# Kernel tuning notes

Hardware: AMD Instinct MI355X
Metric: run time of the kernel (lower is better)

Reference implementation:

```python
import jax, jax.numpy as jnp
import numpy as np

SCALE = 32.0 / 32.0  # alpha / rank
KEEP = 1.0 - 0.05    # dropout keep prob


def setup_inputs() -> dict:
    key = jax.random.key(0)
    kx, kw, ka, kb, km = jax.random.split(key, 5)
    B_, S, D_in, D_out, R = 4, 2048, 4096, 4096, 32
    x = jax.random.normal(kx, (B_, S, D_in), dtype=jnp.float32)
    W = jax.random.normal(kw, (D_out, D_in), dtype=jnp.float32) * (1.0 / np.sqrt(D_in))
    A = jax.random.normal(ka, (D_in, R), dtype=jnp.float32) * (1.0 / np.sqrt(D_in))
    Bm = jax.random.normal(kb, (R, D_out), dtype=jnp.float32) * 0.02
    # deterministic inverted-dropout mask: {0, 1/KEEP}
    drop_mask = (jax.random.uniform(km, (B_, S, D_in)) < KEEP).astype(jnp.float32) / KEEP
    return {"x": x, "W": W, "A": A, "B": Bm, "drop_mask": drop_mask}


def reference(x, W, A, B, drop_mask):
    # base: F.linear(x, W)  -> x @ W.T   [b,s,out]
    base = jnp.einsum("bsi,oi->bso", x, W)
    # lora: dropout(x) @ A @ B, low-rank path (contract rank first)
    lora = jnp.einsum("bsr,ro->bso", jnp.einsum("bsi,ir->bsr", x * drop_mask, A), B)
    return base + SCALE * lora
```

## Files before the change

kernel.cpp:

```cpp
#include <hip/hip_runtime.h>
#include <hip/hip_bf16.h>

typedef short bf16x8 __attribute__((ext_vector_type(8)));
typedef float f32x4  __attribute__((ext_vector_type(4)));

#define DIN  4096
#define DOUT 4096
#define MTOT 8192
#define RNK  32
#define NT   64

union Pk8 { __hip_bfloat16 h[8]; uint4 u; };

__device__ __forceinline__ uint4 pack8(float a0,float a1,float a2,float a3,
                                       float b0,float b1,float b2,float b3){
  Pk8 p;
  p.h[0]=__float2bfloat16(a0); p.h[1]=__float2bfloat16(a1);
  p.h[2]=__float2bfloat16(a2); p.h[3]=__float2bfloat16(a3);
  p.h[4]=__float2bfloat16(b0); p.h[5]=__float2bfloat16(b1);
  p.h[6]=__float2bfloat16(b2); p.h[7]=__float2bfloat16(b3);
  return p.u;
}

__device__ __forceinline__ void gload_lds16(const void* g, void* l){
  __builtin_amdgcn_global_load_lds(
      (const __attribute__((address_space(1))) unsigned int*)g,
      (__attribute__((address_space(3))) unsigned int*)l, 16, 0, 0);
}

#define MFMA(A,B,C) __builtin_amdgcn_mfma_f32_16x16x32_bf16(A,B,C,0,0,0)
#define BAR   asm volatile("s_barrier" ::: "memory")
#define PRIO1 __builtin_amdgcn_s_setprio(1)
#define PRIO0 __builtin_amdgcn_s_setprio(0)

__global__ __launch_bounds__(256) void k_conv_w(const float* __restrict__ W,
                                                __hip_bfloat16* __restrict__ Wb){
  size_t i = ((size_t)blockIdx.x*256 + threadIdx.x) * 8;
  float4 a = *(const float4*)(W + i);
  float4 b = *(const float4*)(W + i + 4);
  *(uint4*)(Wb + i) = pack8(a.x,a.y,a.z,a.w,b.x,b.y,b.z,b.w);
}

__global__ __launch_bounds__(256) void k_conv_ab(const float* __restrict__ A,
                                                 const float* __restrict__ B,
                                                 __hip_bfloat16* __restrict__ At,
                                                 __hip_bfloat16* __restrict__ Bt){
  int idx = blockIdx.x*256 + threadIdx.x;
  if (idx < DIN*RNK){
    int k = idx >> 5, r = idx & 31;
    At[(size_t)r*DIN + k] = __float2bfloat16(A[(size_t)k*RNK + r]);
  } else {
    int j = idx - DIN*RNK;
    int n = j >> 5, k = j & 31;
    Bt[(size_t)n*RNK + k] = __float2bfloat16(B[(size_t)k*DOUT + n]);
  }
}

__global__ __launch_bounds__(256) void k_xt(const float* __restrict__ x,
                                            const float* __restrict__ mk,
                                            const __hip_bfloat16* __restrict__ At,
                                            __hip_bfloat16* __restrict__ xb,
                                            __hip_bfloat16* __restrict__ tb){
  __shared__ __align__(16) __hip_bfloat16 sXM[2][32*64];
  __shared__ __align__(16) __hip_bfloat16 sAT[2][32*64];
  const int t  = threadIdx.x;
  const int bm0 = blockIdx.x * 32;
  const int w = t >> 6, l = t & 63;
  const int mi = w >> 1, ni = w & 1;
  const int row = t >> 3, kc = t & 7;

  f32x4 acc = {0.f,0.f,0.f,0.f};

  auto stage = [&](int nb, int kt){
    const int k0 = kt*64;
    size_t gx = (size_t)(bm0+row)*DIN + k0 + kc*8;
    float4 xa = *(const float4*)(x + gx);
    float4 xc = *(const float4*)(x + gx + 4);
    float4 ma = *(const float4*)(mk + gx);
    float4 mc = *(const float4*)(mk + gx + 4);
    *(uint4*)(xb + gx) = pack8(xa.x,xa.y,xa.z,xa.w,xc.x,xc.y,xc.z,xc.w);
    *(uint4*)(&sXM[nb][t*8]) = pack8(xa.x*ma.x,xa.y*ma.y,xa.z*ma.z,xa.w*ma.w,
                                     xc.x*mc.x,xc.y*mc.y,xc.z*mc.z,xc.w*mc.w);
    gload_lds16(At + (size_t)row*DIN + k0 + kc*8, (void*)&sAT[nb][t*8]);
  };

  stage(0, 0);
  int cur = 0;
  for (int kt = 0; kt < 64; ++kt){
    __syncthreads();
    if (kt + 1 < 64) stage(cur^1, kt+1);
    const __hip_bfloat16* xm = sXM[cur];
    const __hip_bfloat16* at = sAT[cur];
    const int ra = (mi*16 + (l&15))*64 + (l>>4)*8;
    const int rb = (ni*16 + (l&15))*64 + (l>>4)*8;
    acc = MFMA(*(const bf16x8*)(xm+ra),    *(const bf16x8*)(at+rb),    acc);
    acc = MFMA(*(const bf16x8*)(xm+ra+32), *(const bf16x8*)(at+rb+32), acc);
    cur ^= 1;
  }
  const int r0 = bm0 + mi*16 + (l>>4)*4;
  const int c0 = ni*16 + (l&15);
  #pragma unroll
  for (int r = 0; r < 4; ++r)
    tb[(size_t)(r0+r)*RNK + c0] = __float2bfloat16(acc[r]);
}

__global__ __launch_bounds__(512, 2) void k_main2(const __hip_bfloat16* __restrict__ xb,
                                                  const __hip_bfloat16* __restrict__ Wb,
                                                  const __hip_bfloat16* __restrict__ tb,
                                                  const __hip_bfloat16* __restrict__ Bt,
                                                  float* __restrict__ out){
  __shared__ __align__(16) __hip_bfloat16 lds[65536];
  const int tid = threadIdx.x;
  const int l  = tid & 63, w = tid >> 6;
  const int wm = w >> 2,  wn = w & 3;
  const int lr = l & 15;
  const int ch = ((l >> 4) ^ ((l >> 1) & 3)) & 3;
  const int laneA = (wm*128 + lr)*32 + ch*8;
  const int laneB = (wn*64  + lr)*32 + ch*8;
  const int g_row = tid >> 2;
  const int g_ch  = (((tid & 3) ^ ((tid >> 3) & 3))) * 8;

  const int bid = blockIdx.x;
  const int swz = (bid & 7)*64 + (bid >> 3);
  const int bm0 = (swz >> 4) * 256;
  const int bn0 = (swz & 15) * 256;

  f32x4 acc[8][4];

  {
    const __hip_bfloat16* tp = tb + (size_t)(bm0 + wm*128 + lr)*RNK + (l>>4)*8;
    const __hip_bfloat16* bp = Bt + (size_t)(bn0 + wn*64  + lr)*RNK + (l>>4)*8;
    bf16x8 tf[8], bf[4];
    #pragma unroll
    for (int m = 0; m < 8; ++m) tf[m] = *(const bf16x8*)(tp + m*16*RNK);
    #pragma unroll
    for (int n = 0; n < 4; ++n) bf[n] = *(const bf16x8*)(bp + n*16*RNK);
    const f32x4 z = {0.f,0.f,0.f,0.f};
    #pragma unroll
    for (int m = 0; m < 8; ++m)
      #pragma unroll
      for (int n = 0; n < 4; ++n)
        acc[m][n] = MFMA(tf[m], bf[n], z);
  }
  asm volatile("" ::: "memory");

  auto STAGE = [&](int bb, int ab, int kh, int kt){
    const __hip_bfloat16* g = ab ? Wb : xb;
    const int base0 = ab ? bn0 : bm0;
    const int segb  = bb*32768 + ab*16384 + kh*8192;
    #pragma unroll
    for (int i = 0; i < 2; ++i){
      const __hip_bfloat16* src = g + (size_t)(base0 + i*128 + g_row)*DIN
                                    + kt*64 + kh*32 + g_ch;
      gload_lds16(src, (void*)&lds[segb + i*4096 + w*512]);
    }
  };

  STAGE(0,1,0,0); STAGE(0,0,0,0); STAGE(0,1,1,0); STAGE(0,0,1,0);
  STAGE(1,1,0,1); STAGE(1,0,0,1); STAGE(1,1,1,1);
  asm volatile("s_waitcnt vmcnt(6)" ::: "memory");
  BAR;

  #define LDV(off) (*(const bf16x8*)&lds[(off)])

  for (int t = 0; t < NT; ++t){
    const int b   = t & 1;
    const int sA0 = b*32768;
    const int sA1 = b*32768 + 8192;
    const int sB0 = b*32768 + 16384;
    const int sB1 = b*32768 + 24576;
    bf16x8 bk0[4], bk1[4];
    bf16x8 a0, a1, a2, a3;

    a0 = LDV(sA0+laneA);        a1 = LDV(sA0+laneA+512);
    a2 = LDV(sA0+laneA+1024);   a3 = LDV(sA0+laneA+1536);
    #pragma unroll
    for (int n = 0; n < 4; ++n) bk0[n] = LDV(sB0+laneB+n*512);
    if (t+1 < NT) STAGE(b^1, 0, 1, t+1);
    BAR;
    PRIO1;
    #pragma unroll
    for (int n = 0; n < 4; ++n){
      acc[0][n] = MFMA(a0, bk0[n], acc[0][n]);
      acc[1][n] = MFMA(a1, bk0[n], acc[1][n]);
      acc[2][n] = MFMA(a2, bk0[n], acc[2][n]);
      acc[3][n] = MFMA(a3, bk0[n], acc[3][n]);
    }
    PRIO0;
    BAR;

    a0 = LDV(sA0+laneA+2048);   a1 = LDV(sA0+laneA+2560);
    a2 = LDV(sA0+laneA+3072);   a3 = LDV(sA0+laneA+3584);
    #pragma unroll
    for (int n = 0; n < 4; ++n) bk1[n] = LDV(sB1+laneB+n*512);
    if (t+2 < NT) STAGE(b, 1, 0, t+2);
    BAR;
    PRIO1;
    #pragma unroll
    for (int n = 0; n < 4; ++n){
      acc[4][n] = MFMA(a0, bk0[n], acc[4][n]);
      acc[5][n] = MFMA(a1, bk0[n], acc[5][n]);
      acc[6][n] = MFMA(a2, bk0[n], acc[6][n]);
      acc[7][n] = MFMA(a3, bk0[n], acc[7][n]);
    }
    PRIO0;
    BAR;

    a0 = LDV(sA1+laneA);        a1 = LDV(sA1+laneA+512);
    a2 = LDV(sA1+laneA+1024);   a3 = LDV(sA1+laneA+1536);
    if (t+2 < NT) STAGE(b, 0, 0, t+2);
    BAR;
    PRIO1;
    #pragma unroll
    for (int n = 0; n < 4; ++n){
      acc[0][n] = MFMA(a0, bk1[n], acc[0][n]);
      acc[1][n] = MFMA(a1, bk1[n], acc[1][n]);
      acc[2][n] = MFMA(a2, bk1[n], acc[2][n]);
      acc[3][n] = MFMA(a3, bk1[n], acc[3][n]);
    }
    PRIO0;
    BAR;

    a0 = LDV(sA1+laneA+2048);   a1 = LDV(sA1+laneA+2560);
    a2 = LDV(sA1+laneA+3072);   a3 = LDV(sA1+laneA+3584);
    if (t+2 < NT) STAGE(b, 1, 1, t+2);
    BAR;
    PRIO1;
    #pragma unroll
    for (int n = 0; n < 4; ++n){
      acc[4][n] = MFMA(a0, bk1[n], acc[4][n]);
      acc[5][n] = MFMA(a1, bk1[n], acc[5][n]);
      acc[6][n] = MFMA(a2, bk1[n], acc[6][n]);
      acc[7][n] = MFMA(a3, bk1[n], acc[7][n]);
    }
    PRIO0;
    if (t < NT-2)       asm volatile("s_waitcnt vmcnt(6)" ::: "memory");
    else if (t == NT-2) asm volatile("s_waitcnt vmcnt(0)" ::: "memory");
    BAR;
  }

  const int orow = bm0 + wm*128 + (l>>4)*4;
  const int ocol = bn0 + wn*64  + (l&15);
  #pragma unroll
  for (int m = 0; m < 8; ++m)
    #pragma unroll
    for (int n = 0; n < 4; ++n)
      #pragma unroll
      for (int r = 0; r < 4; ++r)
        out[(size_t)(orow + m*16 + r)*DOUT + ocol + n*16] = acc[m][n][r];
  #undef LDV
}

__global__ void fb_t(const float* __restrict__ x, const float* __restrict__ mk,
                     const float* __restrict__ A, float* __restrict__ tf){
  const int m = blockIdx.x, t = threadIdx.x;
  float acc[RNK];
  #pragma unroll
  for (int r = 0; r < RNK; ++r) acc[r] = 0.f;
  for (int k = t; k < DIN; k += 256){
    float xm = x[(size_t)m*DIN + k] * mk[(size_t)m*DIN + k];
    #pragma unroll
    for (int r = 0; r < RNK; ++r) acc[r] += xm * A[(size_t)k*RNK + r];
  }
  #pragma unroll
  for (int r = 0; r < RNK; ++r){
    float v = acc[r];
    for (int o = 32; o; o >>= 1) v += __shfl_down(v, o);
    if ((t & 63) == 0) atomicAdd(&tf[(size_t)m*RNK + r], v);
  }
}

__global__ void fb_out(const float* __restrict__ x, const float* __restrict__ W,
                       const float* __restrict__ B, const float* __restrict__ tf,
                       float* __restrict__ out){
  size_t idx = (size_t)blockIdx.x*256 + threadIdx.x;
  int m = (int)(idx >> 12), n = (int)(idx & 4095);
  float acc = 0.f;
  for (int k = 0; k < DIN; ++k)
    acc += x[(size_t)m*DIN + k] * W[(size_t)n*DIN + k];
  #pragma unroll
  for (int r = 0; r < RNK; ++r)
    acc += tf[(size_t)m*RNK + r] * B[(size_t)r*DOUT + n];
  out[idx] = acc;
}

extern "C" void kernel_launch(void* const* d_in, const int* in_sizes, int n_in,
                              void* d_out, int out_size, void* d_ws, size_t ws_size,
                              hipStream_t stream) {
  const float* x  = (const float*)d_in[0];
  const float* W  = (const float*)d_in[1];
  const float* A  = (const float*)d_in[2];
  const float* B  = (const float*)d_in[3];
  const float* mk = (const float*)d_in[4];
  float* out = (float*)d_out;

  const size_t OFF_XB = 0;
  const size_t OFF_WB = OFF_XB + (size_t)MTOT*DIN*2;
  const size_t OFF_TB = OFF_WB + (size_t)DOUT*DIN*2;
  const size_t OFF_AT = OFF_TB + (size_t)MTOT*RNK*2;
  const size_t OFF_BT = OFF_AT + (size_t)RNK*DIN*2;
  const size_t NEED   = OFF_BT + (size_t)DIN*RNK*2;

  if (ws_size >= NEED){
    char* ws = (char*)d_ws;
    __hip_bfloat16* xb = (__hip_bfloat16*)(ws + OFF_XB);
    __hip_bfloat16* Wb = (__hip_bfloat16*)(ws + OFF_WB);
    __hip_bfloat16* tb = (__hip_bfloat16*)(ws + OFF_TB);
    __hip_bfloat16* At = (__hip_bfloat16*)(ws + OFF_AT);
    __hip_bfloat16* Bt = (__hip_bfloat16*)(ws + OFF_BT);

    k_conv_w <<<(DOUT*(size_t)DIN)/(256*8), 256, 0, stream>>>(W, Wb);
    k_conv_ab<<<(2*DIN*RNK)/256,            256, 0, stream>>>(A, B, At, Bt);
    k_xt     <<<MTOT/32,                    256, 0, stream>>>(x, mk, At, xb, tb);
    k_main2  <<<(MTOT/256)*(DOUT/256),      512, 0, stream>>>(xb, Wb, tb, Bt, out);
  } else {
    float* tf = (float*)d_ws;
    hipMemsetAsync(tf, 0, (size_t)MTOT*RNK*4, stream);
    fb_t  <<<MTOT, 256, 0, stream>>>(x, mk, A, tf);
    fb_out<<<((size_t)MTOT*DOUT)/256, 256, 0, stream>>>(x, W, B, tf, out);
  }
}
```

Before: 358.2 us.

## Split-K rank projection without LDS staging and remap GEMM tiles per XCD

The x·A projection kernel now gives each block 16 rows and splits K across its four waves. Each wave feeds MFMA directly from registers and global memory instead of double-buffered LDS with a barrier every step, and the partial results are reduced through shared memory at the end. This removes 64 barriers per block and doubles the block count for better occupancy. The main GEMM block-to-tile mapping is also changed so each XCD owns two column strips of W, which is meant to improve L2 reuse of W within an XCD while spreading reuse of x across all of them.

After: 411.6 us. +14.9%, slower.

```diff
diff --git a/kernel.cpp b/kernel.cpp
--- a/kernel.cpp
+++ b/kernel.cpp
@@ -10,7 +10,7 @@
 #define RNK  32
 #define NT   64
 
-union Pk8 { __hip_bfloat16 h[8]; uint4 u; };
+union Pk8 { __hip_bfloat16 h[8]; uint4 u; bf16x8 v; };
 
 __device__ __forceinline__ uint4 pack8(float a0,float a1,float a2,float a3,
                                        float b0,float b1,float b2,float b3){
@@ -20,6 +20,15 @@
   p.h[4]=__float2bfloat16(b0); p.h[5]=__float2bfloat16(b1);
   p.h[6]=__float2bfloat16(b2); p.h[7]=__float2bfloat16(b3);
   return p.u;
+}
+__device__ __forceinline__ bf16x8 pack8v(float a0,float a1,float a2,float a3,
+                                         float b0,float b1,float b2,float b3){
+  Pk8 p;
+  p.h[0]=__float2bfloat16(a0); p.h[1]=__float2bfloat16(a1);
+  p.h[2]=__float2bfloat16(a2); p.h[3]=__float2bfloat16(a3);
+  p.h[4]=__float2bfloat16(b0); p.h[5]=__float2bfloat16(b1);
+  p.h[6]=__float2bfloat16(b2); p.h[7]=__float2bfloat16(b3);
+  return p.v;
 }
 
 __device__ __forceinline__ void gload_lds16(const void* g, void* l){
@@ -61,47 +70,48 @@
                                             const __hip_bfloat16* __restrict__ At,
                                             __hip_bfloat16* __restrict__ xb,
                                             __hip_bfloat16* __restrict__ tb){
-  __shared__ __align__(16) __hip_bfloat16 sXM[2][32*64];
-  __shared__ __align__(16) __hip_bfloat16 sAT[2][32*64];
-  const int t  = threadIdx.x;
-  const int bm0 = blockIdx.x * 32;
-  const int w = t >> 6, l = t & 63;
-  const int mi = w >> 1, ni = w & 1;
-  const int row = t >> 3, kc = t & 7;
-
-  f32x4 acc = {0.f,0.f,0.f,0.f};
-
-  auto stage = [&](int nb, int kt){
-    const int k0 = kt*64;
-    size_t gx = (size_t)(bm0+row)*DIN + k0 + kc*8;
-    float4 xa = *(const float4*)(x + gx);
-    float4 xc = *(const float4*)(x + gx + 4);
-    float4 ma = *(const float4*)(mk + gx);
-    float4 mc = *(const float4*)(mk + gx + 4);
-    *(uint4*)(xb + gx) = pack8(xa.x,xa.y,xa.z,xa.w,xc.x,xc.y,xc.z,xc.w);
-    *(uint4*)(&sXM[nb][t*8]) = pack8(xa.x*ma.x,xa.y*ma.y,xa.z*ma.z,xa.w*ma.w,
-                                     xc.x*mc.x,xc.y*mc.y,xc.z*mc.z,xc.w*mc.w);
-    gload_lds16(At + (size_t)row*DIN + k0 + kc*8, (void*)&sAT[nb][t*8]);
-  };
-
-  stage(0, 0);
-  int cur = 0;
-  for (int kt = 0; kt < 64; ++kt){
-    __syncthreads();
-    if (kt + 1 < 64) stage(cur^1, kt+1);
-    const __hip_bfloat16* xm = sXM[cur];
-    const __hip_bfloat16* at = sAT[cur];
-    const int ra = (mi*16 + (l&15))*64 + (l>>4)*8;
-    const int rb = (ni*16 + (l&15))*64 + (l>>4)*8;
-    acc = MFMA(*(const bf16x8*)(xm+ra),    *(const bf16x8*)(at+rb),    acc);
-    acc = MFMA(*(const bf16x8*)(xm+ra+32), *(const bf16x8*)(at+rb+32), acc);
-    cur ^= 1;
-  }
-  const int r0 = bm0 + mi*16 + (l>>4)*4;
-  const int c0 = ni*16 + (l&15);
-  #pragma unroll
-  for (int r = 0; r < 4; ++r)
-    tb[(size_t)(r0+r)*RNK + c0] = __float2bfloat16(acc[r]);
+  __shared__ float sred[4*512];
+  const int t = threadIdx.x, w = t >> 6, l = t & 63;
+  const int r0 = blockIdx.x * 16;
+  const int lane15 = l & 15, kb = l >> 4;
+  const size_t rowbase = (size_t)(r0 + lane15) * DIN;
+  const int kbase = w * 1024;
+
+  f32x4 acc0 = {0.f,0.f,0.f,0.f}, acc1 = {0.f,0.f,0.f,0.f};
+  const __hip_bfloat16* at0 = At + (size_t)lane15*DIN;
+  const __hip_bfloat16* at1 = At + (size_t)(16+lane15)*DIN;
+
+  #pragma unroll 2
+  for (int kt = 0; kt < 32; ++kt){
+    const int k0 = kbase + kt*32 + kb*8;
+    float4 xa = *(const float4*)(x  + rowbase + k0);
+    float4 xc = *(const float4*)(x  + rowbase + k0 + 4);
+    float4 ma = *(const float4*)(mk + rowbase + k0);
+    float4 mc = *(const float4*)(mk + rowbase + k0 + 4);
+    *(uint4*)(xb + rowbase + k0) = pack8(xa.x,xa.y,xa.z,xa.w,xc.x,xc.y,xc.z,xc.w);
+    bf16x8 af = pack8v(xa.x*ma.x,xa.y*ma.y,xa.z*ma.z,xa.w*ma.w,
+                       xc.x*mc.x,xc.y*mc.y,xc.z*mc.z,xc.w*mc.w);
+    bf16x8 b0 = *(const bf16x8*)(at0 + k0);
+    bf16x8 b1 = *(const bf16x8*)(at1 + k0);
+    acc0 = MFMA(af, b0, acc0);
+    acc1 = MFMA(af, b1, acc1);
+  }
+
+  #pragma unroll
+  for (int r = 0; r < 4; ++r){
+    sred[(w*64+l)*8 + r]     = acc0[r];
+    sred[(w*64+l)*8 + 4 + r] = acc1[r];
+  }
+  __syncthreads();
+  #pragma unroll
+  for (int e2 = 0; e2 < 2; ++e2){
+    int e  = t*2 + e2;
+    int el = e >> 3, er = e & 7;
+    float s = sred[el*8+er] + sred[512+el*8+er] + sred[1024+el*8+er] + sred[1536+el*8+er];
+    int col  = (er>>2)*16 + (el & 15);
+    int orow = (el>>4)*4 + (er & 3);
+    tb[(size_t)(r0 + orow)*RNK + col] = __float2bfloat16(s);
+  }
 }
 
 __global__ __launch_bounds__(512, 2) void k_main2(const __hip_bfloat16* __restrict__ xb,
@@ -120,10 +130,10 @@
   const int g_row = tid >> 2;
   const int g_ch  = (((tid & 3) ^ ((tid >> 3) & 3))) * 8;
 
-  const int bid = blockIdx.x;
-  const int swz = (bid & 7)*64 + (bid >> 3);
-  const int bm0 = (swz >> 4) * 256;
-  const int bn0 = (swz & 15) * 256;
+  const int bid  = blockIdx.x;
+  const int xcd  = bid & 7, chunk = bid >> 3;
+  const int bm0  = (chunk & 31) * 256;
+  const int bn0  = (xcd*2 + (chunk >> 5)) * 256;
 
   f32x4 acc[8][4];
 
@@ -311,7 +321,7 @@
 
     k_conv_w <<<(DOUT*(size_t)DIN)/(256*8), 256, 0, stream>>>(W, Wb);
     k_conv_ab<<<(2*DIN*RNK)/256,            256, 0, stream>>>(A, B, At, Bt);
-    k_xt     <<<MTOT/32,                    256, 0, stream>>>(x, mk, At, xb, tb);
+    k_xt     <<<MTOT/16,                    256, 0, stream>>>(x, mk, At, xb, tb);
     k_main2  <<<(MTOT/256)*(DOUT/256),      512, 0, stream>>>(xb, Wb, tb, Bt, out);
   } else {
     float* tf = (float*)d_ws;
```
